# Optimization experiments

Measured on AMD Instinct MI355X. Metric: run time of the kernel, lower is better.

## Reference

```python
import jax, jax.numpy as jnp
import numpy as np

B, T, H, DK, DV, HID = 2, 2048, 6, 256, 256, 2048
EPS = 1e-5


def setup_inputs() -> dict:
    key = jax.random.key(0)
    ks = jax.random.split(key, 12)
    sd = 0.02
    hidden_ab = jax.random.normal(ks[0], (B, T, HID), jnp.float32)
    hidden_g = jax.random.normal(ks[1], (B, T, HID), jnp.float32)
    q = jax.random.normal(ks[2], (B, T, H, DK), jnp.float32)
    k = jax.random.normal(ks[3], (B, T, H, DK), jnp.float32)
    v = jax.random.normal(ks[4], (B, T, H, DV), jnp.float32)
    b_w = jax.random.normal(ks[5], (H, HID), jnp.float32) * sd
    a_w = jax.random.normal(ks[6], (H, HID), jnp.float32) * sd
    g_w = jax.random.normal(ks[7], (H, HID), jnp.float32) * sd
    A_log = jnp.log(jax.random.uniform(ks[8], (H,), jnp.float32, 1.0, 16.0))
    dt = jnp.exp(jax.random.uniform(ks[9], (H,), jnp.float32)
                 * (np.log(0.1) - np.log(0.001)) + np.log(0.001))
    dt = jnp.clip(dt, 1e-4)
    dt_bias = dt + jnp.log(-jnp.expm1(-dt))
    norm_w = jnp.ones((DV,), jnp.float32)
    o_w = jax.random.normal(ks[10], (H, DV, DK), jnp.float32) * sd
    return dict(hidden_ab=hidden_ab, hidden_g=hidden_g, q=q, k=k, v=v,
                b_w=b_w, a_w=a_w, A_log=A_log, dt_bias=dt_bias,
                g_w=g_w, norm_w=norm_w, o_w=o_w)


def _l2norm(x):
    return x * jax.lax.rsqrt(jnp.sum(x * x, axis=-1, keepdims=True) + 1e-6)


def _gated_delta_rule(q, k, v, g, beta):
    # q,k: [B,T,H,DK]; v: [B,T,H,DV]; g,beta: [B,T,H]
    q = _l2norm(q) * (DK ** -0.5)
    k = _l2norm(k)
    # time-major for scan
    qT = jnp.swapaxes(q, 0, 1)
    kT = jnp.swapaxes(k, 0, 1)
    vT = jnp.swapaxes(v, 0, 1)
    gT = jnp.swapaxes(g, 0, 1)
    bT = jnp.swapaxes(beta, 0, 1)

    def step(S, xs):
        qt, kt, vt, gt, bt = xs  # [B,H,*]
        S = S * jnp.exp(gt)[..., None, None]            # gated decay
        pred = jnp.einsum('bhk,bhkv->bhv', kt, S)        # current prediction
        delta = (vt - pred) * bt[..., None]              # beta-scaled error
        S = S + jnp.einsum('bhk,bhv->bhkv', kt, delta)   # delta-rule update
        ot = jnp.einsum('bhk,bhkv->bhv', qt, S)
        return S, ot

    S0 = jnp.zeros((B, H, DK, DV), q.dtype)
    _, oT = jax.lax.scan(step, S0, (qT, kT, vT, gT, bT))
    return jnp.swapaxes(oT, 0, 1)  # [B,T,H,DV]


def reference(hidden_ab, hidden_g, q, k, v, b_w, a_w, A_log, dt_bias, g_w, norm_w, o_w):
    beta = jax.nn.sigmoid(jnp.einsum('bth,nh->btn', hidden_ab, b_w))        # [B,T,H]
    g = -jnp.exp(A_log) * jax.nn.softplus(
        jnp.einsum('bth,nh->btn', hidden_ab, a_w) + dt_bias)                 # [B,T,H]
    o = _gated_delta_rule(q, k, v, g, beta)                                  # [B,T,H,DV]
    # FusedRMSNormSwishGate with per-head scalar gate
    gate = jnp.einsum('bth,nh->btn', hidden_g, g_w)                          # [B,T,H]
    o_n = o * jax.lax.rsqrt(jnp.mean(o * o, axis=-1, keepdims=True) + EPS) * norm_w
    o_n = o_n * (gate * jax.nn.sigmoid(gate))[..., None]
    # GroupLinear per head: head_v_dim -> head_dim
    out = jnp.einsum('bthv,hvd->bthd', o_n, o_w).reshape(B, T, H * DK)
    return out
```

## Files before the change

kernel.cpp:

```cpp
#include <hip/hip_runtime.h>
#include <hip/hip_bf16.h>
#include <math.h>

#define B_ 2
#define T_ 2048
#define H_ 6
#define DK_ 256
#define DV_ 256
#define HID_ 2048
#define C_ 64
#define NC_ 32

typedef __attribute__((ext_vector_type(8))) short short8;
typedef __attribute__((ext_vector_type(4))) float f32x4;

__device__ __forceinline__ unsigned rnebf(float f) {
  unsigned u = __float_as_uint(f);
  return (u + 0x7fffu + ((u >> 16) & 1u)) >> 16;
}
__device__ __forceinline__ unsigned pkbf(float lo, float hi) {
  return rnebf(lo) | (rnebf(hi) << 16);
}
__device__ __forceinline__ float bf2f(unsigned u16v) {
  return __uint_as_float((u16v & 0xffffu) << 16);
}
__device__ __forceinline__ short8 u4_to_s8(uint4 u) {
  union { uint4 u; short8 s; } c; c.u = u; return c.s;
}

__device__ __forceinline__ void gload_lds16(const void* g, void* l) {
  __builtin_amdgcn_global_load_lds(
      (const __attribute__((address_space(1))) unsigned int*)g,
      (__attribute__((address_space(3))) unsigned int*)l, 16, 0, 0);
}

__device__ __forceinline__ short8 buildB(uint2 Pe, uint2 Po, int lg, int c16) {
  const int src0 = ((2 * (lg & 1)) << 4) | c16;
  const int src1 = src0 + 16;
  int e0 = __shfl((int)Pe.x, src0), o0 = __shfl((int)Po.x, src0);
  int e1 = __shfl((int)Pe.y, src0), o1 = __shfl((int)Po.y, src0);
  int e2 = __shfl((int)Pe.x, src1), o2 = __shfl((int)Po.x, src1);
  int e3 = __shfl((int)Pe.y, src1), o3 = __shfl((int)Po.y, src1);
  const bool lo2 = (lg < 2);
  union { int i[4]; short8 s; } u;
  u.i[0] = lo2 ? e0 : o0;
  u.i[1] = lo2 ? e1 : o1;
  u.i[2] = lo2 ? e2 : o2;
  u.i[3] = lo2 ? e3 : o3;
  return u.s;
}

__global__ __launch_bounds__(256, 1) void gdn_projnorm_kernel(
    const float* __restrict__ hab, const float* __restrict__ hg,
    const float* __restrict__ b_w, const float* __restrict__ a_w,
    const float* __restrict__ g_w, const float* __restrict__ A_log,
    const float* __restrict__ dt_bias,
    float* __restrict__ beta_o, float* __restrict__ g_o,
    float* __restrict__ sgate_o,
    const float* __restrict__ q, const float* __restrict__ k,
    float* __restrict__ sq, float* __restrict__ sk) {
  const int tid = threadIdx.x;
  const int lane = tid & 63;
  const int wid = tid >> 6;

  if (blockIdx.x >= B_ * T_) {
    const int gw = (blockIdx.x - B_ * T_) * 4 + wid;
    const float4 qv = *(const float4*)(q + (size_t)gw * DK_ + lane * 4);
    const float4 kv = *(const float4*)(k + (size_t)gw * DK_ + lane * 4);
    float sums_q = qv.x * qv.x + qv.y * qv.y + qv.z * qv.z + qv.w * qv.w;
    float sums_k = kv.x * kv.x + kv.y * kv.y + kv.z * kv.z + kv.w * kv.w;
#pragma unroll
    for (int m = 1; m < 64; m <<= 1) {
      sums_q += __shfl_xor(sums_q, m);
      sums_k += __shfl_xor(sums_k, m);
    }
    if (lane == 0) {
      sq[gw] = rsqrtf(sums_q + 1e-6f) * 0.0625f;
      sk[gw] = rsqrtf(sums_k + 1e-6f);
    }
    return;
  }

  const int bt = blockIdx.x;
  const float* h1 = hab + (size_t)bt * HID_ + tid * 8;
  const float* h2 = hg + (size_t)bt * HID_ + tid * 8;
  const float4 xa = *(const float4*)(h1);
  const float4 xb = *(const float4*)(h1 + 4);
  const float4 ya = *(const float4*)(h2);
  const float4 yb = *(const float4*)(h2 + 4);

  float4 wv0[18], wv1[18];
#pragma unroll
  for (int n = 0; n < 6; ++n) {
    const float* wp = b_w + n * HID_ + tid * 8;
    wv0[n] = *(const float4*)(wp);
    wv1[n] = *(const float4*)(wp + 4);
  }
#pragma unroll
  for (int n = 0; n < 6; ++n) {
    const float* wp = a_w + n * HID_ + tid * 8;
    wv0[6 + n] = *(const float4*)(wp);
    wv1[6 + n] = *(const float4*)(wp + 4);
  }
#pragma unroll
  for (int n = 0; n < 6; ++n) {
    const float* wp = g_w + n * HID_ + tid * 8;
    wv0[12 + n] = *(const float4*)(wp);
    wv1[12 + n] = *(const float4*)(wp + 4);
  }

  float part[18];
#pragma unroll
  for (int n = 0; n < 12; ++n) {
    part[n] = xa.x * wv0[n].x + xa.y * wv0[n].y + xa.z * wv0[n].z +
              xa.w * wv0[n].w + xb.x * wv1[n].x + xb.y * wv1[n].y +
              xb.z * wv1[n].z + xb.w * wv1[n].w;
  }
#pragma unroll
  for (int n = 12; n < 18; ++n) {
    part[n] = ya.x * wv0[n].x + ya.y * wv0[n].y + ya.z * wv0[n].z +
              ya.w * wv0[n].w + yb.x * wv1[n].x + yb.y * wv1[n].y +
              yb.z * wv1[n].z + yb.w * wv1[n].w;
  }

  __shared__ float red[18][4];
#pragma unroll
  for (int i = 0; i < 18; ++i) {
    float x = part[i];
    x += __shfl_xor(x, 1);
    x += __shfl_xor(x, 2);
    x += __shfl_xor(x, 4);
    x += __shfl_xor(x, 8);
    x += __shfl_xor(x, 16);
    x += __shfl_xor(x, 32);
    if (lane == 0) red[i][wid] = x;
  }
  __syncthreads();

  if (tid < 18) {
    const float s = red[tid][0] + red[tid][1] + red[tid][2] + red[tid][3];
    if (tid < 6) {
      beta_o[(size_t)bt * H_ + tid] = 1.f / (1.f + __expf(-s));
    } else if (tid < 12) {
      const int n = tid - 6;
      const float x = s + dt_bias[n];
      const float sp = (x > 20.f) ? x : log1pf(__expf(x));
      g_o[(size_t)bt * H_ + n] = -__expf(A_log[n]) * sp;
    } else {
      const int n = tid - 12;
      sgate_o[(size_t)bt * H_ + n] = s / (1.f + __expf(-s));
    }
  }
}

__global__ __launch_bounds__(256) void gdn_cum_kernel(
    const float* __restrict__ g, float* __restrict__ Gc,
    float* __restrict__ lam) {
  const int bh = blockIdx.x;
  const int b = bh / H_, h = bh - b * H_;
  const int w = threadIdx.x >> 6, l = threadIdx.x & 63;
  for (int it = 0; it < 8; ++it) {
    const int nc = it * 4 + w;
    const int tg = nc * C_ + l;
    const size_t srow = ((size_t)b * T_ + tg) * H_ + h;
    float val = g[srow];
#pragma unroll
    for (int ofs = 1; ofs < 64; ofs <<= 1) {
      const float o = __shfl_up(val, ofs);
      if (l >= ofs) val += o;
    }
    Gc[(bh * NC_ + nc) * C_ + l] = val;
    if (l == 63) lam[bh * NC_ + nc] = __expf(val);
  }
}

__device__ __forceinline__ int swz4(int row, int c4) {
  return row * 256 + (((c4) ^ ((row >> 2) & 7)) << 2);
}
__device__ __forceinline__ int swzi(int row, int c) {
  return row * 256 + ((((c) >> 2) ^ ((row >> 2) & 7)) << 2) + ((c) & 3);
}

__global__ __launch_bounds__(256) void gdn_prep_kernel(
    const float* __restrict__ q, const float* __restrict__ k,
    const float* __restrict__ v, const float* __restrict__ beta,
    const float* __restrict__ sq, const float* __restrict__ sk,
    const float* __restrict__ Gc, uint2* __restrict__ wUp,
    ushort* __restrict__ wWp, ushort* __restrict__ wMp,
    ushort* __restrict__ wQd, ushort* __restrict__ wkT,
    const float* __restrict__ o_w, ushort* __restrict__ owT) {
  __shared__ __attribute__((aligned(16))) char smem[158720];

  const int bid = blockIdx.x;
  const int tid = threadIdx.x;

  if (bid >= 512) {
    const int b2 = bid - 512;
    const int h2 = b2 >> 2;
    const int db = (b2 & 3) * 64;
    ushort* t = (ushort*)smem;
#pragma unroll
    for (int it = 0; it < 16; ++it) {
      const int v2 = it * 16 + (tid >> 4);
      const int dl = 4 * (tid & 15);
      const float4 x =
          *(const float4*)&o_w[((size_t)h2 * 256 + v2) * 256 + db + dl];
      t[(dl + 0) * 264 + v2] = (ushort)rnebf(x.x);
      t[(dl + 1) * 264 + v2] = (ushort)rnebf(x.y);
      t[(dl + 2) * 264 + v2] = (ushort)rnebf(x.z);
      t[(dl + 3) * 264 + v2] = (ushort)rnebf(x.w);
    }
    __syncthreads();
#pragma unroll
    for (int it = 0; it < 8; ++it) {
      const int idx = it * 256 + tid;
      const int d = idx >> 5;
      const int vv = (idx & 31) * 8;
      uint4 o;
      o.x = *(uint*)&t[d * 264 + vv + 0]; o.y = *(uint*)&t[d * 264 + vv + 2];
      o.z = *(uint*)&t[d * 264 + vv + 4]; o.w = *(uint*)&t[d * 264 + vv + 6];
      *(uint4*)&owT[((size_t)h2 * 256 + db + d) * 256 + vv] = o;
    }
    return;
  }

  const int bhx = bid & 15;
  if (bhx >= B_ * H_) return;
  const int nc = bid >> 4;
  const int bh = bhx;
  const int b = bh / H_, h = bh - b * H_;
  const int w = tid >> 6, l = tid & 63;
  const int lg = l >> 4, c16 = l & 15;
  const int cidx = bh * NC_ + nc;

  float* r1 = (float*)smem;
  ushort* knB = (ushort*)smem;
  ushort* qnB = (ushort*)(smem + 32768);
  float* r2 = (float*)(smem + 65536);
  float* AlT = (float*)(smem + 131072);
  ushort* Msc = (ushort*)(smem + 148480);
  float* bG = (float*)(smem + 157696);
  float* bB = bG + 64;
  float* bSc = bG + 128;
  float* bWl = bG + 192;

  const size_t srow0 = ((size_t)b * T_ + nc * C_) * H_ + h;
  if (tid < C_) {
    const float gv = Gc[cidx * C_ + tid];
    bG[tid] = gv;
    const float bb = beta[srow0 + (size_t)tid * H_];
    bB[tid] = bb;
    bSc[tid] = __expf(Gc[cidx * C_ + C_ - 1] - gv);
    bWl[tid] = bb * __expf(gv);
  }
  __syncthreads();

#pragma unroll
  for (int rr = 0; rr < 16; ++rr) {
    const int row = rr * 4 + w;
    const size_t g0 = (srow0 + (size_t)row * H_) * DK_;
    const float skr = sk[srow0 + (size_t)row * H_];
    const float sqr = sq[srow0 + (size_t)row * H_];
    float4 kv = *(const float4*)(k + g0 + 4 * l);
    float4 qv = *(const float4*)(q + g0 + 4 * l);
    kv.x *= skr; kv.y *= skr; kv.z *= skr; kv.w *= skr;
    qv.x *= sqr; qv.y *= sqr; qv.z *= sqr; qv.w *= sqr;
    const int boff = row * 512 + ((8 * l) ^ ((row & 7) << 4));
    uint2 pk_, pq_;
    pk_.x = pkbf(kv.x, kv.y); pk_.y = pkbf(kv.z, kv.w);
    pq_.x = pkbf(qv.x, qv.y); pq_.y = pkbf(qv.z, qv.w);
    *(uint2*)((char*)knB + boff) = pk_;
    *(uint2*)((char*)qnB + boff) = pq_;
    const float qe = __expf(bG[row]);
    uint2 oq;
    oq.x = pkbf(qv.x * qe, qv.y * qe);
    oq.y = pkbf(qv.z * qe, qv.w * qe);
    *(uint2*)&wQd[(srow0 + (size_t)row * H_) * DK_ + 4 * l] = oq;
  }
  __syncthreads();

  {
    const int xorv = (c16 & 7) << 4;
    const int rowA = 16 * w + c16;
    uint4 aq[8], ak[8];
#pragma unroll
    for (int kt = 0; kt < 8; ++kt) {
      const int coff = (64 * kt + 16 * lg) ^ xorv;
      aq[kt] = *(const uint4*)((char*)qnB + rowA * 512 + coff);
      ak[kt] = *(const uint4*)((char*)knB + rowA * 512 + coff);
    }
    f32x4 accm[4], acca[4];
#pragma unroll
    for (int nt = 0; nt < 4; ++nt) {
      accm[nt] = (f32x4){0.f, 0.f, 0.f, 0.f};
      acca[nt] = (f32x4){0.f, 0.f, 0.f, 0.f};
    }
#pragma unroll
    for (int nt = 0; nt < 4; ++nt) {
      const int rowB = 16 * nt + c16;
#pragma unroll
      for (int kt = 0; kt < 8; ++kt) {
        const uint4 bk =
            *(const uint4*)((char*)knB + rowB * 512 + ((64 * kt + 16 * lg) ^ xorv));
        const short8 bkf = u4_to_s8(bk);
        accm[nt] = __builtin_amdgcn_mfma_f32_16x16x32_bf16(u4_to_s8(aq[kt]),
                                                           bkf, accm[nt], 0, 0, 0);
        acca[nt] = __builtin_amdgcn_mfma_f32_16x16x32_bf16(u4_to_s8(ak[kt]),
                                                           bkf, acca[nt], 0, 0, 0);
      }
    }
#pragma unroll
    for (int nt = 0; nt < 4; ++nt) {
#pragma unroll
      for (int r = 0; r < 4; ++r) {
        const int t = 16 * w + 4 * lg + r;
        const int i = 16 * nt + c16;
        const float eg = __expf(bG[t] - bG[i]);
        Msc[t * 72 + i] = (ushort)((i <= t) ? rnebf(accm[nt][r] * eg) : 0u);
        AlT[i * 68 + t] = (i < t) ? bB[t] * eg * acca[nt][r] : 0.f;
      }
    }
  }
  {
    const int d = tid;
#pragma unroll
    for (int e = 0; e < 8; ++e) {
      float vj[8];
#pragma unroll
      for (int j = 0; j < 8; ++j) {
        const int t = 8 * e + j;
        const float kv = bf2f(*(const ushort*)((char*)knB + t * 512 +
                                               ((2 * d) ^ ((t & 7) << 4))));
        vj[j] = kv;
        r2[swzi(t, d)] = kv * bWl[t];
      }
      uint4 o;
      o.x = pkbf(vj[0] * bSc[8 * e + 0], vj[1] * bSc[8 * e + 1]);
      o.y = pkbf(vj[2] * bSc[8 * e + 2], vj[3] * bSc[8 * e + 3]);
      o.z = pkbf(vj[4] * bSc[8 * e + 4], vj[5] * bSc[8 * e + 5]);
      o.w = pkbf(vj[6] * bSc[8 * e + 6], vj[7] * bSc[8 * e + 7]);
      *(uint4*)&wkT[((size_t)cidx * 256 + d) * C_ + 8 * e] = o;
    }
  }
  __syncthreads();

  {
    const int row = tid >> 2;
#pragma unroll
    for (int e = 0; e < 2; ++e) {
      const int col = ((tid & 3) * 2 + e) * 8;
      *(uint4*)&wMp[(size_t)cidx * C_ * C_ + row * C_ + col] =
          *(const uint4*)&Msc[row * 72 + col];
    }
  }
#pragma unroll
  for (int rr = 0; rr < 16; ++rr) {
    const int row = rr * 4 + w;
    const float bbr = bB[row];
    const size_t g0 = (srow0 + (size_t)row * H_) * DV_;
    float4 vv = *(const float4*)(v + g0 + 4 * l);
    vv.x *= bbr; vv.y *= bbr; vv.z *= bbr; vv.w *= bbr;
    *(float4*)&r1[swz4(row, l)] = vv;
  }
  __syncthreads();

#pragma unroll
  for (int tb = 0; tb < 8; ++tb) {
    float xu[8], xw[8];
#pragma unroll
    for (int e = 0; e < 8; ++e) {
      xu[e] = r1[swzi(8 * tb + e, tid)];
      xw[e] = r2[swzi(8 * tb + e, tid)];
    }
    for (int i = 0; i < 8 * tb; ++i) {
      const float xui = r1[swzi(i, tid)];
      const float xwi = r2[swzi(i, tid)];
      float av[8];
      *(float4*)&av[0] = *(float4*)&AlT[i * 68 + 8 * tb];
      *(float4*)&av[4] = *(float4*)&AlT[i * 68 + 8 * tb + 4];
#pragma unroll
      for (int e = 0; e < 8; ++e) {
        xu[e] = fmaf(-av[e], xui, xu[e]);
        xw[e] = fmaf(-av[e], xwi, xw[e]);
      }
    }
#pragma unroll
    for (int e = 1; e < 8; ++e)
#pragma unroll
      for (int m = 0; m < 7; ++m)
        if (m < e) {
          const float am = AlT[(8 * tb + m) * 68 + 8 * tb + e];
          xu[e] = fmaf(-am, xu[m], xu[e]);
          xw[e] = fmaf(-am, xw[m], xw[e]);
        }
#pragma unroll
    for (int e = 0; e < 8; ++e) {
      r1[swzi(8 * tb + e, tid)] = xu[e];
      r2[swzi(8 * tb + e, tid)] = xw[e];
    }
  }
  {
    ushort* wb = wWp + (size_t)cidx * C_ * 256;
    for (int row = 0; row < C_; ++row)
      wb[row * 256 + tid] = (ushort)rnebf(r2[swzi(row, tid)]);
    const int cbw = tid >> 4, c16s = tid & 15;
#pragma unroll
    for (int mt = 0; mt < 4; ++mt) {
#pragma unroll
      for (int lgi = 0; lgi < 4; ++lgi) {
        const int r0 = 16 * mt + 4 * lgi;
        uint2 val;
        val.x = pkbf(r1[swzi(r0 + 0, tid)], r1[swzi(r0 + 1, tid)]);
        val.y = pkbf(r1[swzi(r0 + 2, tid)], r1[swzi(r0 + 3, tid)]);
        wUp[(((size_t)cidx * 16 + cbw) * 4 + mt) * 64 + (lgi << 4) + c16s] = val;
      }
    }
  }
}

__global__ __launch_bounds__(128, 1) void gdn_seq_kernel(
    const ushort* __restrict__ wkT, const ushort* __restrict__ wWp,
    const uint2* __restrict__ wUp, const float* __restrict__ lam,
    uint2* __restrict__ wDP, uint2* __restrict__ wSP) {
  const int bid = blockIdx.x;
  const int cb = bid >> 4, bhx = bid & 15;
  if (bhx >= B_ * H_) return;
  const int bh = bhx;
  const int tid = threadIdx.x;
  const int kh = tid >> 6, l = tid & 63;
  const int lg = l >> 4, c16 = l & 15;
  const int xorv = (c16 & 7) << 4;

  __shared__ ushort sW[2][16384];
  __shared__ ushort sK[2][16384];
  __shared__ uint2 sU[2][256];
  __shared__ f32x4 sX[2][4][64];
  __shared__ float sLam[NC_];

  auto stage = [&](int pp, int cidx2) {
    const char* gw_ = (const char*)(wWp + (size_t)cidx2 * 16384);
#pragma unroll
    for (int j = 0; j < 16; ++j) {
      const int i = kh * 16 + j;
      const int row = 2 * i + (l >> 5);
      const int colb = ((l & 31) * 16) ^ ((row & 7) << 4);
      gload_lds16(gw_ + row * 512 + colb, (char*)&sW[pp][0] + i * 1024);
    }
    const char* gk_ = (const char*)(wkT + (size_t)cidx2 * 16384);
#pragma unroll
    for (int j = 0; j < 16; ++j) {
      const int i = kh * 16 + j;
      const int row = 8 * i + (l >> 3);
      const int colb = ((l & 7) * 16) ^ ((row & 7) << 4);
      gload_lds16(gk_ + row * 128 + colb, (char*)&sK[pp][0] + i * 1024);
    }
    const char* gu_ = (const char*)wUp + ((size_t)cidx2 * 16 + cb) * 2048;
    gload_lds16(gu_ + kh * 1024 + l * 16, (char*)&sU[pp][0] + kh * 1024);
  };

  f32x4 S[8];
#pragma unroll
  for (int m2 = 0; m2 < 8; ++m2) S[m2] = (f32x4){0.f, 0.f, 0.f, 0.f};

  stage(0, bh * NC_ + 0);
  stage(1, bh * NC_ + 1);
  if (tid < NC_) sLam[tid] = lam[bh * NC_ + tid];
  asm volatile("s_waitcnt lgkmcnt(0)" ::: "memory");
  __builtin_amdgcn_sched_barrier(0);
  __builtin_amdgcn_s_barrier();
  __builtin_amdgcn_sched_barrier(0);

  for (int nc = 0; nc < NC_; ++nc) {
    const int pp = nc & 1;
    const int cidx = bh * NC_ + nc;
    if (nc == 0)
      asm volatile("s_waitcnt vmcnt(33)" ::: "memory");
    else if (nc == NC_ - 1)
      asm volatile("s_waitcnt vmcnt(5)" ::: "memory");
    else
      asm volatile("s_waitcnt vmcnt(38)" ::: "memory");
    __builtin_amdgcn_sched_barrier(0);
    __builtin_amdgcn_s_barrier();
    __builtin_amdgcn_sched_barrier(0);

    uint2 P[8];
#pragma unroll
    for (int m2 = 0; m2 < 8; ++m2) {
      P[m2].x = pkbf(S[m2][0], S[m2][1]);
      P[m2].y = pkbf(S[m2][2], S[m2][3]);
    }
    {
      uint4* sp4 = (uint4*)(wSP + (((size_t)cidx * 16 + cb) * 64 + l) * 16 +
                            kh * 8);
#pragma unroll
      for (int i = 0; i < 4; ++i) {
        uint4 o; o.x = P[2 * i].x; o.y = P[2 * i].y;
        o.z = P[2 * i + 1].x; o.w = P[2 * i + 1].y;
        sp4[i] = o;
      }
    }

    f32x4 pe[4], po[4];
#pragma unroll
    for (int mt = 0; mt < 4; ++mt) {
      pe[mt] = (f32x4){0.f, 0.f, 0.f, 0.f};
      po[mt] = (f32x4){0.f, 0.f, 0.f, 0.f};
    }
    const char* sWb = (const char*)&sW[pp][0];
#pragma unroll
    for (int ktl = 0; ktl < 4; ++ktl) {
      const int kt = kh * 4 + ktl;
      const short8 Bf = buildB(P[2 * ktl], P[2 * ktl + 1], lg, c16);
      const int colb = (64 * kt + 16 * lg) ^ xorv;
#pragma unroll
      for (int mt = 0; mt < 4; ++mt) {
        const uint4 aw = *(const uint4*)(sWb + (16 * mt + c16) * 512 + colb);
        if (ktl & 1)
          po[mt] = __builtin_amdgcn_mfma_f32_16x16x32_bf16(u4_to_s8(aw), Bf,
                                                           po[mt], 0, 0, 0);
        else
          pe[mt] = __builtin_amdgcn_mfma_f32_16x16x32_bf16(u4_to_s8(aw), Bf,
                                                           pe[mt], 0, 0, 0);
      }
    }
    f32x4 pl[4];
#pragma unroll
    for (int mt = 0; mt < 4; ++mt) {
      pl[mt] = pe[mt] + po[mt];
      sX[kh][mt][l] = pl[mt];
    }
    asm volatile("s_waitcnt lgkmcnt(0)" ::: "memory");
    __builtin_amdgcn_sched_barrier(0);
    __builtin_amdgcn_s_barrier();
    __builtin_amdgcn_sched_barrier(0);

    uint2 DP[4];
#pragma unroll
    for (int mt = 0; mt < 4; ++mt) {
      const f32x4 pr = sX[kh ^ 1][mt][l];
      const uint2 uu = sU[pp][mt * 64 + l];
      const float d0 = bf2f(uu.x) - (pl[mt][0] + pr[0]);
      const float d1 = bf2f(uu.x >> 16) - (pl[mt][1] + pr[1]);
      const float d2 = bf2f(uu.y) - (pl[mt][2] + pr[2]);
      const float d3 = bf2f(uu.y >> 16) - (pl[mt][3] + pr[3]);
      DP[mt].x = pkbf(d0, d1);
      DP[mt].y = pkbf(d2, d3);
    }
    {
      uint4* dp4 = (uint4*)(wDP + (((size_t)cidx * 16 + cb) * 64 + l) * 4);
      uint4 od;
      if (kh == 0) { od.x = DP[0].x; od.y = DP[0].y; od.z = DP[1].x; od.w = DP[1].y; }
      else         { od.x = DP[2].x; od.y = DP[2].y; od.z = DP[3].x; od.w = DP[3].y; }
      dp4[kh] = od;
    }
    const float lamC = sLam[nc];
#pragma unroll
    for (int m2 = 0; m2 < 8; ++m2) {
      S[m2][0] *= lamC; S[m2][1] *= lamC; S[m2][2] *= lamC; S[m2][3] *= lamC;
    }
    const char* sKb = (const char*)&sK[pp][0];
#pragma unroll
    for (int kt2 = 0; kt2 < 2; ++kt2) {
      const short8 Bd = buildB(DP[2 * kt2], DP[2 * kt2 + 1], lg, c16);
      const int colb = (64 * kt2 + 16 * lg) ^ xorv;
#pragma unroll
      for (int m2 = 0; m2 < 8; ++m2) {
        const int m2g = kh * 8 + m2;
        const uint4 ak = *(const uint4*)(sKb + (16 * m2g + c16) * 128 + colb);
        S[m2] = __builtin_amdgcn_mfma_f32_16x16x32_bf16(u4_to_s8(ak), Bd,
                                                        S[m2], 0, 0, 0);
      }
    }
    __builtin_amdgcn_sched_barrier(0);
    __builtin_amdgcn_s_barrier();
    __builtin_amdgcn_sched_barrier(0);
    if (nc + 2 < NC_) stage(pp, cidx + 2);
    __builtin_amdgcn_sched_barrier(0);
  }
}

__global__ __launch_bounds__(256) void gdn_ofin_kernel(
    const ushort* __restrict__ wQd, const ushort* __restrict__ wMp,
    const uint2* __restrict__ wDP, const uint2* __restrict__ wSP,
    const float* __restrict__ sgate, const float* __restrict__ norm_w,
    const ushort* __restrict__ owT, float* __restrict__ out) {
  const int slot = blockIdx.x;
  const int bhx = slot & 15;
  if (bhx >= B_ * H_) return;
  const int nc = slot >> 4;
  const int bh = bhx;
  const int cidx = bh * NC_ + nc;
  const int b = bh / H_, h = bh - b * H_;
  const int tid = threadIdx.x;
  const int w = tid >> 6, l = tid & 63;
  const int lg = l >> 4, c16 = l & 15;
  const size_t t0 = (size_t)b * T_ + nc * C_;

  __shared__ ushort onl[64 * 256];
  __shared__ float red[64][4];
  __shared__ float rowf[64];

  f32x4 acc[4][4];
#pragma unroll
  for (int mt = 0; mt < 4; ++mt)
#pragma unroll
    for (int nt = 0; nt < 4; ++nt) acc[mt][nt] = (f32x4){0.f, 0.f, 0.f, 0.f};

#pragma unroll
  for (int nt = 0; nt < 4; ++nt) {
    const int cbwq = 4 * w + nt;
    uint2 SPl[16];
    const uint4* sp4 =
        (const uint4*)(wSP + (((size_t)cidx * 16 + cbwq) * 64 + l) * 16);
#pragma unroll
    for (int i = 0; i < 8; ++i) {
      const uint4 t4 = sp4[i];
      SPl[2 * i].x = t4.x; SPl[2 * i].y = t4.y;
      SPl[2 * i + 1].x = t4.z; SPl[2 * i + 1].y = t4.w;
    }
#pragma unroll
    for (int kt = 0; kt < 8; ++kt) {
      const short8 Bf = buildB(SPl[2 * kt], SPl[2 * kt + 1], lg, c16);
#pragma unroll
      for (int mt = 0; mt < 4; ++mt) {
        const uint4 aq = *(const uint4*)&wQd[((t0 + 16 * mt + c16) * H_ + h) *
                                                 (size_t)DK_ +
                                             32 * kt + 8 * lg];
        acc[mt][nt] = __builtin_amdgcn_mfma_f32_16x16x32_bf16(
            u4_to_s8(aq), Bf, acc[mt][nt], 0, 0, 0);
      }
    }
  }
  const ushort* Mb = wMp + (size_t)cidx * C_ * C_;
#pragma unroll
  for (int nt = 0; nt < 4; ++nt) {
    const int cbwq = 4 * w + nt;
    uint2 DPl[4];
    {
      const uint4* dp4 =
          (const uint4*)(wDP + (((size_t)cidx * 16 + cbwq) * 64 + l) * 4);
      const uint4 a0 = dp4[0], a1 = dp4[1];
      DPl[0].x = a0.x; DPl[0].y = a0.y; DPl[1].x = a0.z; DPl[1].y = a0.w;
      DPl[2].x = a1.x; DPl[2].y = a1.y; DPl[3].x = a1.z; DPl[3].y = a1.w;
    }
#pragma unroll
    for (int kt2 = 0; kt2 < 2; ++kt2) {
      const short8 Bf = buildB(DPl[2 * kt2], DPl[2 * kt2 + 1], lg, c16);
#pragma unroll
      for (int mt = 0; mt < 4; ++mt) {
        const uint4 am =
            *(const uint4*)&Mb[(16 * mt + c16) * C_ + 32 * kt2 + 8 * lg];
        acc[mt][nt] = __builtin_amdgcn_mfma_f32_16x16x32_bf16(
            u4_to_s8(am), Bf, acc[mt][nt], 0, 0, 0);
      }
    }
  }

  float ss[4][4];
#pragma unroll
  for (int mt = 0; mt < 4; ++mt)
#pragma unroll
    for (int r = 0; r < 4; ++r) {
      float s = acc[mt][0][r] * acc[mt][0][r];
      s = fmaf(acc[mt][1][r], acc[mt][1][r], s);
      s = fmaf(acc[mt][2][r], acc[mt][2][r], s);
      s = fmaf(acc[mt][3][r], acc[mt][3][r], s);
      s += __shfl_xor(s, 1);
      s += __shfl_xor(s, 2);
      s += __shfl_xor(s, 4);
      s += __shfl_xor(s, 8);
      ss[mt][r] = s;
    }
  if (c16 == 0) {
#pragma unroll
    for (int mt = 0; mt < 4; ++mt)
#pragma unroll
      for (int r = 0; r < 4; ++r) red[16 * mt + 4 * lg + r][w] = ss[mt][r];
  }
  __syncthreads();
  if (tid < 64) {
    const float ms =
        (red[tid][0] + red[tid][1] + red[tid][2] + red[tid][3]) * (1.f / DV_);
    const float sg = sgate[(t0 + tid) * H_ + h];
    rowf[tid] = rsqrtf(ms + 1e-5f) * sg;
  }
  __syncthreads();

  {
    char* onb = (char*)onl;
#pragma unroll
    for (int mt = 0; mt < 4; ++mt) {
      float rf[4];
#pragma unroll
      for (int r = 0; r < 4; ++r) rf[r] = rowf[16 * mt + 4 * lg + r];
#pragma unroll
      for (int nt = 0; nt < 4; ++nt) {
        const int c = (4 * w + nt) * 16 + c16;
        const float nwv = norm_w[c];
#pragma unroll
        for (int r = 0; r < 4; ++r) {
          const int row = 16 * mt + 4 * lg + r;
          const float v = acc[mt][nt][r] * rf[r] * nwv;
          *(ushort*)(onb + row * 512 + ((2 * c) ^ ((row & 7) << 4))) =
              (ushort)rnebf(v);
        }
      }
    }
  }
  __syncthreads();

  f32x4 acc2[4][4];
#pragma unroll
  for (int mt = 0; mt < 4; ++mt)
#pragma unroll
    for (int nt2 = 0; nt2 < 4; ++nt2)
      acc2[mt][nt2] = (f32x4){0.f, 0.f, 0.f, 0.f};
  {
    const char* onb = (const char*)onl;
#pragma unroll
    for (int kt = 0; kt < 8; ++kt) {
      uint4 af[4];
#pragma unroll
      for (int mt = 0; mt < 4; ++mt)
        af[mt] = *(const uint4*)(onb + (16 * mt + c16) * 512 +
                                 ((64 * kt + 16 * lg) ^ ((c16 & 7) << 4)));
#pragma unroll
      for (int nt2 = 0; nt2 < 4; ++nt2) {
        const uint4 bf = *(const uint4*)&owT[((size_t)h * 256 +
                                              (4 * w + nt2) * 16 + c16) *
                                                 256 +
                                             32 * kt + 8 * lg];
#pragma unroll
        for (int mt = 0; mt < 4; ++mt)
          acc2[mt][nt2] = __builtin_amdgcn_mfma_f32_16x16x32_bf16(
              u4_to_s8(af[mt]), u4_to_s8(bf), acc2[mt][nt2], 0, 0, 0);
      }
    }
  }
#pragma unroll
  for (int mt = 0; mt < 4; ++mt)
#pragma unroll
    for (int nt2 = 0; nt2 < 4; ++nt2)
#pragma unroll
      for (int r = 0; r < 4; ++r)
        out[((t0 + 16 * mt + 4 * lg + r) * H_ + h) * (size_t)DK_ +
            (4 * w + nt2) * 16 + c16] = acc2[mt][nt2][r];
}

extern "C" void kernel_launch(void* const* d_in, const int* in_sizes, int n_in,
                              void* d_out, int out_size, void* d_ws,
                              size_t ws_size, hipStream_t stream) {
  const float* hab = (const float*)d_in[0];
  const float* hg = (const float*)d_in[1];
  const float* q = (const float*)d_in[2];
  const float* k = (const float*)d_in[3];
  const float* v = (const float*)d_in[4];
  const float* b_w = (const float*)d_in[5];
  const float* a_w = (const float*)d_in[6];
  const float* A_log = (const float*)d_in[7];
  const float* dt_bias = (const float*)d_in[8];
  const float* g_w = (const float*)d_in[9];
  const float* norm_w = (const float*)d_in[10];
  const float* o_w = (const float*)d_in[11];
  float* out = (float*)d_out;

  float* ws = (float*)d_ws;
  const size_t NBT = (size_t)B_ * T_ * H_;
  float* w_beta = ws;
  float* w_g = ws + NBT;
  float* w_sg = ws + 2 * NBT;
  float* w_sq = ws + 3 * NBT;
  float* w_sk = ws + 4 * NBT;
  float* w_G = ws + 5 * NBT;
  float* w_lam = ws + 7 * NBT;
  ushort* w_Qd = (ushort*)(ws + 7 * NBT + 1024);
  ushort* w_kT = w_Qd + (size_t)12582912;
  ushort* w_W = w_kT + (size_t)6291456;
  ushort* w_M = w_W + (size_t)6291456;
  uint2* w_U = (uint2*)(w_M + (size_t)1572864);
  uint2* w_DP = w_U + (size_t)1572864;
  uint2* w_SP = w_DP + (size_t)1572864;
  ushort* w_owT = (ushort*)(w_SP + (size_t)6291456);

  hipLaunchKernelGGL(gdn_projnorm_kernel,
                     dim3(B_ * T_ + B_ * T_ * H_ / 4), dim3(256), 0, stream,
                     hab, hg, b_w, a_w, g_w, A_log, dt_bias, w_beta, w_g,
                     w_sg, q, k, w_sq, w_sk);
  hipLaunchKernelGGL(gdn_cum_kernel, dim3(B_ * H_), dim3(256), 0, stream,
                     w_g, w_G, w_lam);
  hipLaunchKernelGGL(gdn_prep_kernel, dim3(512 + 24), dim3(256), 0, stream,
                     q, k, v, w_beta, w_sq, w_sk, w_G, w_U, w_W, w_M,
                     w_Qd, w_kT, o_w, w_owT);
  hipLaunchKernelGGL(gdn_seq_kernel, dim3(256), dim3(128), 0, stream,
                     w_kT, w_W, w_U, w_lam, w_DP, w_SP);
  hipLaunchKernelGGL(gdn_ofin_kernel, dim3(512), dim3(256), 0, stream,
                     w_Qd, w_M, w_DP, w_SP, w_sg, norm_w, w_owT, out);
}
```

Measured before the change: 265.4 us.

## Keep projection weights in registers and process 16 rows per block in projnorm

The projection part of the first kernel now assigns one wavefront per weight matrix (b, a, g), loads that wavefront's six weight rows into registers once, and streams 16 token rows per block with double-buffered row loads. Before, every token row had its own block that reloaded all 18 weight rows. The change cuts weight traffic and block count and removes the LDS reduction and syncthreads. The cost is that one of the four wavefronts sits idle, register pressure is high (96 float4s), and there are fewer blocks to hide latency.

```diff
diff --git a/kernel.cpp b/kernel.cpp
--- a/kernel.cpp
+++ b/kernel.cpp
@@ -63,8 +63,8 @@
   const int lane = tid & 63;
   const int wid = tid >> 6;
 
-  if (blockIdx.x >= B_ * T_) {
-    const int gw = (blockIdx.x - B_ * T_) * 4 + wid;
+  if (blockIdx.x >= 256) {
+    const int gw = (blockIdx.x - 256) * 4 + wid;
     const float4 qv = *(const float4*)(q + (size_t)gw * DK_ + lane * 4);
     const float4 kv = *(const float4*)(k + (size_t)gw * DK_ + lane * 4);
     float sums_q = qv.x * qv.x + qv.y * qv.y + qv.z * qv.z + qv.w * qv.w;
@@ -81,75 +81,78 @@
     return;
   }
 
-  const int bt = blockIdx.x;
-  const float* h1 = hab + (size_t)bt * HID_ + tid * 8;
-  const float* h2 = hg + (size_t)bt * HID_ + tid * 8;
-  const float4 xa = *(const float4*)(h1);
-  const float4 xb = *(const float4*)(h1 + 4);
-  const float4 ya = *(const float4*)(h2);
-  const float4 yb = *(const float4*)(h2 + 4);
-
-  float4 wv0[18], wv1[18];
+  if (wid == 3) return;
+  const int bt0 = blockIdx.x * 16;
+  const float* wbase = (wid == 0) ? b_w : (wid == 1) ? a_w : g_w;
+  const float* hbase = (wid == 2) ? hg : hab;
+
+  float4 wv[6][8];
+#pragma unroll
+  for (int n = 0; n < 6; ++n)
+#pragma unroll
+    for (int j = 0; j < 8; ++j)
+      wv[n][j] = *(const float4*)(wbase + n * HID_ + j * 256 + 4 * lane);
+
+  float alog[6], dtb[6];
 #pragma unroll
   for (int n = 0; n < 6; ++n) {
-    const float* wp = b_w + n * HID_ + tid * 8;
-    wv0[n] = *(const float4*)(wp);
-    wv1[n] = *(const float4*)(wp + 4);
-  }
-#pragma unroll
-  for (int n = 0; n < 6; ++n) {
-    const float* wp = a_w + n * HID_ + tid * 8;
-    wv0[6 + n] = *(const float4*)(wp);
-    wv1[6 + n] = *(const float4*)(wp + 4);
-  }
-#pragma unroll
-  for (int n = 0; n < 6; ++n) {
-    const float* wp = g_w + n * HID_ + tid * 8;
-    wv0[12 + n] = *(const float4*)(wp);
-    wv1[12 + n] = *(const float4*)(wp + 4);
-  }
-
-  float part[18];
-#pragma unroll
-  for (int n = 0; n < 12; ++n) {
-    part[n] = xa.x * wv0[n].x + xa.y * wv0[n].y + xa.z * wv0[n].z +
-              xa.w * wv0[n].w + xb.x * wv1[n].x + xb.y * wv1[n].y +
-              xb.z * wv1[n].z + xb.w * wv1[n].w;
-  }
-#pragma unroll
-  for (int n = 12; n < 18; ++n) {
-    part[n] = ya.x * wv0[n].x + ya.y * wv0[n].y + ya.z * wv0[n].z +
-              ya.w * wv0[n].w + yb.x * wv1[n].x + yb.y * wv1[n].y +
-              yb.z * wv1[n].z + yb.w * wv1[n].w;
-  }
-
-  __shared__ float red[18][4];
-#pragma unroll
-  for (int i = 0; i < 18; ++i) {
-    float x = part[i];
-    x += __shfl_xor(x, 1);
-    x += __shfl_xor(x, 2);
-    x += __shfl_xor(x, 4);
-    x += __shfl_xor(x, 8);
-    x += __shfl_xor(x, 16);
-    x += __shfl_xor(x, 32);
-    if (lane == 0) red[i][wid] = x;
-  }
-  __syncthreads();
-
-  if (tid < 18) {
-    const float s = red[tid][0] + red[tid][1] + red[tid][2] + red[tid][3];
-    if (tid < 6) {
-      beta_o[(size_t)bt * H_ + tid] = 1.f / (1.f + __expf(-s));
-    } else if (tid < 12) {
-      const int n = tid - 6;
-      const float x = s + dt_bias[n];
-      const float sp = (x > 20.f) ? x : log1pf(__expf(x));
-      g_o[(size_t)bt * H_ + n] = -__expf(A_log[n]) * sp;
-    } else {
-      const int n = tid - 12;
-      sgate_o[(size_t)bt * H_ + n] = s / (1.f + __expf(-s));
-    }
+    alog[n] = A_log[n];
+    dtb[n] = dt_bias[n];
+  }
+
+  auto prow = [&](const float4* h, int r) {
+    float s[6];
+#pragma unroll
+    for (int n = 0; n < 6; ++n) {
+      float acc = h[0].x * wv[n][0].x + h[0].y * wv[n][0].y +
+                  h[0].z * wv[n][0].z + h[0].w * wv[n][0].w;
+#pragma unroll
+      for (int j = 1; j < 8; ++j)
+        acc += h[j].x * wv[n][j].x + h[j].y * wv[n][j].y +
+               h[j].z * wv[n][j].z + h[j].w * wv[n][j].w;
+#pragma unroll
+      for (int m = 1; m < 64; m <<= 1) acc += __shfl_xor(acc, m);
+      s[n] = acc;
+    }
+    if (lane == 0) {
+      const size_t base = (size_t)(bt0 + r) * H_;
+      if (wid == 0) {
+#pragma unroll
+        for (int n = 0; n < 6; ++n)
+          beta_o[base + n] = 1.f / (1.f + __expf(-s[n]));
+      } else if (wid == 1) {
+#pragma unroll
+        for (int n = 0; n < 6; ++n) {
+          const float x = s[n] + dtb[n];
+          const float sp = (x > 20.f) ? x : log1pf(__expf(x));
+          g_o[base + n] = -__expf(alog[n]) * sp;
+        }
+      } else {
+#pragma unroll
+        for (int n = 0; n < 6; ++n)
+          sgate_o[base + n] = s[n] / (1.f + __expf(-s[n]));
+      }
+    }
+  };
+
+  float4 ha[8], hb[8];
+#pragma unroll
+  for (int j = 0; j < 8; ++j)
+    ha[j] = *(const float4*)(hbase + (size_t)bt0 * HID_ + j * 256 + 4 * lane);
+
+  for (int r = 0; r < 16; r += 2) {
+#pragma unroll
+    for (int j = 0; j < 8; ++j)
+      hb[j] = *(const float4*)(hbase + (size_t)(bt0 + r + 1) * HID_ +
+                               j * 256 + 4 * lane);
+    prow(ha, r);
+    if (r + 2 < 16) {
+#pragma unroll
+      for (int j = 0; j < 8; ++j)
+        ha[j] = *(const float4*)(hbase + (size_t)(bt0 + r + 2) * HID_ +
+                                 j * 256 + 4 * lane);
+    }
+    prow(hb, r + 1);
   }
 }
 
@@ -783,7 +786,7 @@
   ushort* w_owT = (ushort*)(w_SP + (size_t)6291456);
 
   hipLaunchKernelGGL(gdn_projnorm_kernel,
-                     dim3(B_ * T_ + B_ * T_ * H_ / 4), dim3(256), 0, stream,
+                     dim3(256 + B_ * T_ * H_ / 4), dim3(256), 0, stream,
                      hab, hg, b_w, a_w, g_w, A_log, dt_bias, w_beta, w_g,
                      w_sg, q, k, w_sq, w_sk);
   hipLaunchKernelGGL(gdn_cum_kernel, dim3(B_ * H_), dim3(256), 0, stream,
```

Result: no change. 264.8 us (-0.2%).
